# Kernel optimization log

Hardware: AMD Instinct MI355X
Metric: run time of the kernel (lower is better)

## Reference

```python
import jax, jax.numpy as jnp
import numpy as np

N_NODES = 100000
N_EDGES = 1600000
D_IN = 64
D_OUT = 64
BN_EPS = 1e-5


def setup_inputs() -> dict:
    key = jax.random.key(0)
    k1, k2, k3 = jax.random.split(key, 3)
    x = jax.random.normal(k1, (N_NODES, D_IN), dtype=jnp.float32)
    edge_index = jax.random.randint(k2, (2, N_EDGES), 0, N_NODES, dtype=jnp.int64)
    # GCNConv linear weight [out, in], glorot-ish scale
    W = jax.random.normal(k3, (D_OUT, D_IN), dtype=jnp.float32) / np.sqrt(D_IN)
    b = jnp.zeros((D_OUT,), dtype=jnp.float32)
    gamma = jnp.ones((D_OUT,), dtype=jnp.float32)
    beta = jnp.zeros((D_OUT,), dtype=jnp.float32)
    return {"x": x, "edge_index": edge_index, "W": W, "b": b, "gamma": gamma, "beta": beta}


def reference(x, edge_index, W, b, gamma, beta):
    # --- GCNConv: h = x @ W^T, propagate with sym-normalized adjacency + self-loops ---
    h = x @ W.T  # [N, D_OUT]
    src, tgt = edge_index[0], edge_index[1]
    # degree at target nodes, +1 for self-loop
    deg = jax.ops.segment_sum(jnp.ones((src.shape[0],), h.dtype), tgt,
                              num_segments=N_NODES) + 1.0  # [N]
    dinv = jax.lax.rsqrt(deg)
    norm = dinv[src] * dinv[tgt]  # [E]
    # gather -> scale -> scatter-add; self-loop contribution is h / deg
    agg = jax.ops.segment_sum(h[src] * norm[:, None], tgt, num_segments=N_NODES)
    out = agg + h * (1.0 / deg)[:, None] + b  # [N, D_OUT]
    # --- BatchNorm1d (training-mode batch statistics, biased variance) ---
    mean = out.mean(axis=0)
    var = out.var(axis=0)
    y = gamma * (out - mean) * jax.lax.rsqrt(var + BN_EPS) + beta
    # --- ReLU (dropout = identity in eval) ---
    return jax.nn.relu(y)
```

## Files before the change

### kernel.cpp

```cpp
#include <hip/hip_runtime.h>
#include <stdint.h>

#define N_NODES_C 100000
#define N_EDGES_C 1600000
#define DIM 64
#define BN_EPS_C 1e-5f
#define BSH 7
#define NB 782
#define CH 8192

__device__ __forceinline__ int ld_idx(const void* p, int is64, size_t i) {
    if (is64) return (int)((const long long*)p)[i];
    return ((const int*)p)[i];
}

__device__ __forceinline__ float bflo(unsigned int u) {
    return __uint_as_float(u << 16);
}
__device__ __forceinline__ float bfhi(unsigned int u) {
    return __uint_as_float(u & 0xFFFF0000u);
}
__device__ __forceinline__ unsigned short f2bf(float f) {
    unsigned int u = __float_as_uint(f);
    return (unsigned short)((u + 0x7FFF + ((u >> 16) & 1)) >> 16);
}

__global__ void probe_kernel(const unsigned int* __restrict__ p, int* __restrict__ flag) {
    if (threadIdx.x == 0 && blockIdx.x == 0) {
        int is64 = 1;
        for (int i = 1; i < 64; i += 2) {
            if (p[i] != 0u) { is64 = 0; break; }
        }
        *flag = is64;
    }
}

__global__ __launch_bounds__(256) void hist_kernel(const void* __restrict__ ei,
                                                   const int* __restrict__ flag,
                                                   int* __restrict__ bucket_cnt) {
    __shared__ int hist[NB];
    for (int i = threadIdx.x; i < NB; i += 256) hist[i] = 0;
    __syncthreads();
    int is64 = *flag;
    int stride = gridDim.x * blockDim.x;
    for (int e = blockIdx.x * blockDim.x + threadIdx.x; e < N_EDGES_C; e += stride) {
        int tg = ld_idx(ei, is64, (size_t)N_EDGES_C + e);
        atomicAdd(&hist[tg >> BSH], 1);
    }
    __syncthreads();
    for (int i = threadIdx.x; i < NB; i += 256) {
        int c = hist[i];
        if (c) atomicAdd(&bucket_cnt[i], c);
    }
}

__global__ __launch_bounds__(1024) void bucketscan_kernel(const int* __restrict__ bucket_cnt,
                                                          int* __restrict__ bucket_base,
                                                          int* __restrict__ bucket_cursor) {
    __shared__ int s[1024];
    int t = threadIdx.x;
    int v = (t < NB) ? bucket_cnt[t] : 0;
    s[t] = v;
    __syncthreads();
    for (int off = 1; off < 1024; off <<= 1) {
        int u = (t >= off) ? s[t - off] : 0;
        __syncthreads();
        s[t] += u;
        __syncthreads();
    }
    if (t < NB) {
        int excl = s[t] - v;
        bucket_base[t] = excl;
        bucket_cursor[t] = excl;
    }
}

__global__ __launch_bounds__(256) void binscatter_kernel(const void* __restrict__ ei,
                                                         const int* __restrict__ flag,
                                                         int* __restrict__ bucket_cursor,
                                                         unsigned int* __restrict__ csr) {
    __shared__ int hist[NB];
    __shared__ int base[NB];
    int is64 = *flag;
    int e0 = blockIdx.x * CH;
    int eend = min(e0 + CH, N_EDGES_C);
    for (int i = threadIdx.x; i < NB; i += 256) hist[i] = 0;
    __syncthreads();
    for (int e = e0 + threadIdx.x; e < eend; e += 256) {
        int tg = ld_idx(ei, is64, (size_t)N_EDGES_C + e);
        atomicAdd(&hist[tg >> BSH], 1);
    }
    __syncthreads();
    for (int i = threadIdx.x; i < NB; i += 256) {
        int c = hist[i];
        base[i] = c ? atomicAdd(&bucket_cursor[i], c) : 0;
        hist[i] = 0;
    }
    __syncthreads();
    for (int e = e0 + threadIdx.x; e < eend; e += 256) {
        int s  = ld_idx(ei, is64, (size_t)e);
        int tg = ld_idx(ei, is64, (size_t)N_EDGES_C + e);
        int b  = tg >> BSH;
        int tl = tg & 127;
        int pos = base[b] + atomicAdd(&hist[b], 1);
        csr[pos] = ((unsigned int)tl << 17) | (unsigned int)s;
    }
}

__global__ __launch_bounds__(256) void sort_kernel(const unsigned int* __restrict__ csr,
                                                   const int* __restrict__ bucket_base,
                                                   const int* __restrict__ bucket_cnt,
                                                   int* __restrict__ csr2,
                                                   int* __restrict__ rowbase,
                                                   float* __restrict__ dinv) {
    __shared__ int cnt[128];
    __shared__ int sbase[129];
    __shared__ int cur[128];
    int bk = blockIdx.x;
    int t = threadIdx.x;
    if (t < 128) cnt[t] = 0;
    __syncthreads();
    int base = bucket_base[bk], n = bucket_cnt[bk];
    for (int i = t; i < n; i += 256) {
        atomicAdd(&cnt[csr[base + i] >> 17], 1);
    }
    __syncthreads();
    if (t == 0) {
        int run = 0;
        for (int k = 0; k < 128; ++k) { sbase[k] = run; run += cnt[k]; }
        sbase[128] = run;
    }
    __syncthreads();
    if (t < 128) {
        cur[t] = base + sbase[t];
        int node = (bk << BSH) + t;
        if (node < N_NODES_C) {
            rowbase[node] = base + sbase[t];
            float d = (float)(cnt[t] + 1);
            dinv[node] = rsqrtf(d);
        }
    }
    if (bk == 0 && t == 0) rowbase[N_NODES_C] = N_EDGES_C;
    __syncthreads();
    for (int i = t; i < n; i += 256) {
        unsigned int v = csr[base + i];
        int tl = v >> 17;
        int pos = atomicAdd(&cur[tl], 1);
        csr2[pos] = (int)(v & 0x1FFFF);
    }
}

__global__ __launch_bounds__(256) void gemm_kernel(const float* __restrict__ x,
                                                   const float* __restrict__ W,
                                                   const float* __restrict__ dinv,
                                                   unsigned short* __restrict__ hs) {
    __shared__ float Wl[DIM * 65];
    __shared__ float xs[32][DIM];
    int t = threadIdx.x;
    for (int i = t; i < DIM * DIM; i += 256) {
        Wl[(i >> 6) * 65 + (i & 63)] = W[i];
    }
    int r0 = blockIdx.x * 32;
    for (int i = t; i < 32 * DIM; i += 256) {
        int row = i >> 6, col = i & 63;
        int r = r0 + row;
        xs[row][col] = (r < N_NODES_C) ? x[(size_t)r * DIM + col] : 0.0f;
    }
    __syncthreads();
    int wv = t >> 6, c = t & 63;
    for (int it = 0; it < 8; ++it) {
        int rl = it * 4 + wv;
        int r = r0 + rl;
        float acc = 0.0f;
#pragma unroll
        for (int k = 0; k < DIM; ++k) acc += xs[rl][k] * Wl[c * 65 + k];
        if (r < N_NODES_C) hs[(size_t)r * DIM + c] = f2bf(acc * dinv[r]);
    }
}

__global__ __launch_bounds__(256) void gather_kernel(const int* __restrict__ csr2,
                                                     const int* __restrict__ rowbase,
                                                     const float* __restrict__ dinv,
                                                     const unsigned int* __restrict__ hs2,
                                                     const float* __restrict__ b_,
                                                     float2* __restrict__ out,
                                                     float* __restrict__ sums,
                                                     float* __restrict__ sumsq) {
    int lane = threadIdx.x & 63;
    int half = lane >> 5;
    int c2 = lane & 31;
    int wid = blockIdx.x * (blockDim.x >> 6) + (threadIdx.x >> 6);
    int nw = gridDim.x * (blockDim.x >> 6);
    float2 bb = ((const float2*)b_)[c2];
    float s0a = 0.0f, q0a = 0.0f, s1a = 0.0f, q1a = 0.0f;
    for (int p = wid; p < N_NODES_C / 2; p += nw) {
        int t = 2 * p + half;
        int base = rowbase[t];
        int n = rowbase[t + 1] - base;
        float dt = dinv[t];
        float a0 = 0.0f, a1 = 0.0f;
        int j = 0;
        for (; j + 8 <= n; j += 8) {
            int sA = csr2[base + j + 0];
            int sB = csr2[base + j + 1];
            int sC = csr2[base + j + 2];
            int sD = csr2[base + j + 3];
            int sE = csr2[base + j + 4];
            int sF = csr2[base + j + 5];
            int sG = csr2[base + j + 6];
            int sH = csr2[base + j + 7];
            unsigned int uA = hs2[(size_t)sA * 32 + c2];
            unsigned int uB = hs2[(size_t)sB * 32 + c2];
            unsigned int uC = hs2[(size_t)sC * 32 + c2];
            unsigned int uD = hs2[(size_t)sD * 32 + c2];
            unsigned int uE = hs2[(size_t)sE * 32 + c2];
            unsigned int uF = hs2[(size_t)sF * 32 + c2];
            unsigned int uG = hs2[(size_t)sG * 32 + c2];
            unsigned int uH = hs2[(size_t)sH * 32 + c2];
            a0 += bflo(uA); a1 += bfhi(uA);
            a0 += bflo(uB); a1 += bfhi(uB);
            a0 += bflo(uC); a1 += bfhi(uC);
            a0 += bflo(uD); a1 += bfhi(uD);
            a0 += bflo(uE); a1 += bfhi(uE);
            a0 += bflo(uF); a1 += bfhi(uF);
            a0 += bflo(uG); a1 += bfhi(uG);
            a0 += bflo(uH); a1 += bfhi(uH);
        }
        for (; j + 2 <= n; j += 2) {
            int sA = csr2[base + j + 0];
            int sB = csr2[base + j + 1];
            unsigned int uA = hs2[(size_t)sA * 32 + c2];
            unsigned int uB = hs2[(size_t)sB * 32 + c2];
            a0 += bflo(uA); a1 += bfhi(uA);
            a0 += bflo(uB); a1 += bfhi(uB);
        }
        if (j < n) {
            int s = csr2[base + j];
            unsigned int u = hs2[(size_t)s * 32 + c2];
            a0 += bflo(u); a1 += bfhi(u);
        }
        unsigned int ut = hs2[(size_t)t * 32 + c2];
        a0 = fmaf(a0 + bflo(ut), dt, bb.x);
        a1 = fmaf(a1 + bfhi(ut), dt, bb.y);
        out[(size_t)t * 32 + c2] = make_float2(a0, a1);
        s0a += a0; q0a += a0 * a0;
        s1a += a1; q1a += a1 * a1;
    }
    __shared__ float r0[256], r1[256], r2[256], r3[256];
    r0[threadIdx.x] = s0a; r1[threadIdx.x] = q0a;
    r2[threadIdx.x] = s1a; r3[threadIdx.x] = q1a;
    __syncthreads();
    if (threadIdx.x < 32) {
        float S0 = 0, Q0 = 0, S1 = 0, Q1 = 0;
        for (int k = threadIdx.x; k < 256; k += 32) {
            S0 += r0[k]; Q0 += r1[k]; S1 += r2[k]; Q1 += r3[k];
        }
        unsafeAtomicAdd(&sums[2 * threadIdx.x], S0);
        unsafeAtomicAdd(&sums[2 * threadIdx.x + 1], S1);
        unsafeAtomicAdd(&sumsq[2 * threadIdx.x], Q0);
        unsafeAtomicAdd(&sumsq[2 * threadIdx.x + 1], Q1);
    }
}

__global__ void bnparam_kernel(const float* __restrict__ sums,
                               const float* __restrict__ sumsq,
                               const float* __restrict__ gamma,
                               const float* __restrict__ beta,
                               float* __restrict__ scale,
                               float* __restrict__ shift) {
    int c = threadIdx.x;
    if (c < DIM) {
        float m = sums[c] * (1.0f / N_NODES_C);
        float var = sumsq[c] * (1.0f / N_NODES_C) - m * m;
        float sc = gamma[c] * rsqrtf(var + BN_EPS_C);
        scale[c] = sc;
        shift[c] = beta[c] - m * sc;
    }
}

__global__ __launch_bounds__(256) void bnrelu_kernel(float4* __restrict__ out,
                                                     const float* __restrict__ scale,
                                                     const float* __restrict__ shift) {
    const int n4 = N_NODES_C * (DIM / 4);
    int stride = gridDim.x * blockDim.x;
    for (int i = blockIdx.x * blockDim.x + threadIdx.x; i < n4; i += stride) {
        int cb = (i & 15) * 4;
        float4 v = out[i];
        v.x = fmaxf(fmaf(v.x, scale[cb + 0], shift[cb + 0]), 0.0f);
        v.y = fmaxf(fmaf(v.y, scale[cb + 1], shift[cb + 1]), 0.0f);
        v.z = fmaxf(fmaf(v.z, scale[cb + 2], shift[cb + 2]), 0.0f);
        v.w = fmaxf(fmaf(v.w, scale[cb + 3], shift[cb + 3]), 0.0f);
        out[i] = v;
    }
}

extern "C" void kernel_launch(void* const* d_in, const int* in_sizes, int n_in,
                              void* d_out, int out_size, void* d_ws, size_t ws_size,
                              hipStream_t stream) {
    const float* x     = (const float*)d_in[0];
    const void*  ei    = d_in[1];
    const float* W     = (const float*)d_in[2];
    const float* b     = (const float*)d_in[3];
    const float* gamma = (const float*)d_in[4];
    const float* beta  = (const float*)d_in[5];
    float* out = (float*)d_out;

    char* ws = (char*)d_ws;
    int*   flag          = (int*)(ws + 0);
    int*   bucket_cnt    = (int*)(ws + 256);
    int*   bucket_base   = (int*)(ws + 3584);
    int*   bucket_cursor = (int*)(ws + 6912);
    float* dinv          = (float*)(ws + 10240);
    int*   rowbase       = (int*)(ws + 410240);
    float* sums          = (float*)(ws + 810496);
    float* sumsq         = (float*)(ws + 810752);
    float* scale         = (float*)(ws + 811008);
    float* shift         = (float*)(ws + 811264);
    unsigned int* csr    = (unsigned int*)(ws + 811520);
    int*   csr2          = (int*)(ws + 7211520);
    unsigned short* hs   = (unsigned short*)(ws + 13611520);

    hipMemsetAsync(bucket_cnt, 0, NB * sizeof(int), stream);
    hipMemsetAsync(sums, 0, 512, stream);

    probe_kernel<<<1, 64, 0, stream>>>((const unsigned int*)ei, flag);
    hist_kernel<<<256, 256, 0, stream>>>(ei, flag, bucket_cnt);
    bucketscan_kernel<<<1, 1024, 0, stream>>>(bucket_cnt, bucket_base, bucket_cursor);
    binscatter_kernel<<<(N_EDGES_C + CH - 1) / CH, 256, 0, stream>>>(ei, flag,
                                                                    bucket_cursor, csr);
    sort_kernel<<<NB, 256, 0, stream>>>(csr, bucket_base, bucket_cnt, csr2,
                                        rowbase, dinv);
    gemm_kernel<<<(N_NODES_C + 31) / 32, 256, 0, stream>>>(x, W, dinv, hs);
    gather_kernel<<<2048, 256, 0, stream>>>(csr2, rowbase, dinv,
                                            (const unsigned int*)hs, b,
                                            (float2*)out, sums, sumsq);
    bnparam_kernel<<<1, 64, 0, stream>>>(sums, sumsq, gamma, beta, scale, shift);
    bnrelu_kernel<<<1024, 256, 0, stream>>>((float4*)out, scale, shift);
}
```

Baseline: 257.5 us.

## Tile gather by source-node range across rows for cache locality

The sort kernel now sub-buckets each target row's edges into 7 source-node tiles (source>>14), storing per-node tile offsets. Each half-wave of the gather kernel handles 7 consecutive rows and walks all of them tile by tile, so concurrently running waves read source features from the same ~16K-node window and hit cache more often. The workspace layout also changes: csr and hs now share the same memory, which is safe only because the sort kernel consumes csr before the gemm kernel writes hs. In exchange, the gather loops are shorter per tile with more boundary overhead, and the per-node offset array grows to 8 entries per node.

```diff
diff --git a/kernel.cpp b/kernel.cpp
--- a/kernel.cpp
+++ b/kernel.cpp
@@ -8,6 +8,8 @@
 #define BSH 7
 #define NB 782
 #define CH 8192
+#define NT 7
+#define RPS 7
 
 __device__ __forceinline__ int ld_idx(const void* p, int is64, size_t i) {
     if (is64) return (int)((const long long*)p)[i];
@@ -111,41 +113,45 @@
                                                    const int* __restrict__ bucket_base,
                                                    const int* __restrict__ bucket_cnt,
                                                    int* __restrict__ csr2,
-                                                   int* __restrict__ rowbase,
+                                                   int* __restrict__ tilebase,
                                                    float* __restrict__ dinv) {
-    __shared__ int cnt[128];
-    __shared__ int sbase[129];
-    __shared__ int cur[128];
+    __shared__ int cnt[128 * NT];
+    __shared__ int sbase[128 * NT + 1];
+    __shared__ int cur[128 * NT];
     int bk = blockIdx.x;
     int t = threadIdx.x;
-    if (t < 128) cnt[t] = 0;
+    for (int i = t; i < 128 * NT; i += 256) cnt[i] = 0;
     __syncthreads();
     int base = bucket_base[bk], n = bucket_cnt[bk];
     for (int i = t; i < n; i += 256) {
-        atomicAdd(&cnt[csr[base + i] >> 17], 1);
+        unsigned int v = csr[base + i];
+        int key = (int)(v >> 17) * NT + (int)((v & 0x1FFFF) >> 14);
+        atomicAdd(&cnt[key], 1);
     }
     __syncthreads();
     if (t == 0) {
         int run = 0;
-        for (int k = 0; k < 128; ++k) { sbase[k] = run; run += cnt[k]; }
-        sbase[128] = run;
-    }
-    __syncthreads();
+        for (int k = 0; k < 128 * NT; ++k) { sbase[k] = run; run += cnt[k]; }
+        sbase[128 * NT] = run;
+    }
+    __syncthreads();
+    for (int i = t; i < 128 * NT; i += 256) cur[i] = base + sbase[i];
     if (t < 128) {
-        cur[t] = base + sbase[t];
         int node = (bk << BSH) + t;
         if (node < N_NODES_C) {
-            rowbase[node] = base + sbase[t];
-            float d = (float)(cnt[t] + 1);
-            dinv[node] = rsqrtf(d);
-        }
-    }
-    if (bk == 0 && t == 0) rowbase[N_NODES_C] = N_EDGES_C;
+#pragma unroll
+            for (int k = 0; k < NT; ++k)
+                tilebase[node * 8 + k] = base + sbase[t * NT + k];
+            tilebase[node * 8 + NT] = base + sbase[t * NT + NT];
+            int d = sbase[t * NT + NT] - sbase[t * NT];
+            dinv[node] = rsqrtf((float)(d + 1));
+        }
+    }
     __syncthreads();
     for (int i = t; i < n; i += 256) {
         unsigned int v = csr[base + i];
-        int tl = v >> 17;
-        int pos = atomicAdd(&cur[tl], 1);
+        int key = (int)(v >> 17) * NT + (int)((v & 0x1FFFF) >> 14);
+        int pos = atomicAdd(&cur[key], 1);
         csr2[pos] = (int)(v & 0x1FFFF);
     }
 }
@@ -179,7 +185,7 @@
 }
 
 __global__ __launch_bounds__(256) void gather_kernel(const int* __restrict__ csr2,
-                                                     const int* __restrict__ rowbase,
+                                                     const int* __restrict__ tilebase,
                                                      const float* __restrict__ dinv,
                                                      const unsigned int* __restrict__ hs2,
                                                      const float* __restrict__ b_,
@@ -189,62 +195,62 @@
     int lane = threadIdx.x & 63;
     int half = lane >> 5;
     int c2 = lane & 31;
-    int wid = blockIdx.x * (blockDim.x >> 6) + (threadIdx.x >> 6);
-    int nw = gridDim.x * (blockDim.x >> 6);
+    int slot = (blockIdx.x * 4 + (threadIdx.x >> 6)) * 2 + half;
+    int row0 = slot * RPS;
+    float a0[RPS], a1[RPS];
+#pragma unroll
+    for (int r = 0; r < RPS; ++r) { a0[r] = 0.0f; a1[r] = 0.0f; }
+
+    for (int tt = 0; tt < NT; ++tt) {
+        int sr[RPS], er[RPS];
+#pragma unroll
+        for (int r = 0; r < RPS; ++r) {
+            int node = row0 + r;
+            bool valid = node < N_NODES_C;
+            sr[r] = valid ? tilebase[node * 8 + tt] : 0;
+            er[r] = valid ? tilebase[node * 8 + tt + 1] : 0;
+        }
+#pragma unroll
+        for (int r = 0; r < RPS; ++r) {
+            float x0 = a0[r], x1 = a1[r];
+            int j = sr[r], e = er[r];
+            for (; j + 4 <= e; j += 4) {
+                int sA = csr2[j + 0];
+                int sB = csr2[j + 1];
+                int sC = csr2[j + 2];
+                int sD = csr2[j + 3];
+                unsigned int uA = hs2[(size_t)sA * 32 + c2];
+                unsigned int uB = hs2[(size_t)sB * 32 + c2];
+                unsigned int uC = hs2[(size_t)sC * 32 + c2];
+                unsigned int uD = hs2[(size_t)sD * 32 + c2];
+                x0 += bflo(uA); x1 += bfhi(uA);
+                x0 += bflo(uB); x1 += bfhi(uB);
+                x0 += bflo(uC); x1 += bfhi(uC);
+                x0 += bflo(uD); x1 += bfhi(uD);
+            }
+            for (; j < e; ++j) {
+                int s = csr2[j];
+                unsigned int u = hs2[(size_t)s * 32 + c2];
+                x0 += bflo(u); x1 += bfhi(u);
+            }
+            a0[r] = x0; a1[r] = x1;
+        }
+    }
+
     float2 bb = ((const float2*)b_)[c2];
     float s0a = 0.0f, q0a = 0.0f, s1a = 0.0f, q1a = 0.0f;
-    for (int p = wid; p < N_NODES_C / 2; p += nw) {
-        int t = 2 * p + half;
-        int base = rowbase[t];
-        int n = rowbase[t + 1] - base;
-        float dt = dinv[t];
-        float a0 = 0.0f, a1 = 0.0f;
-        int j = 0;
-        for (; j + 8 <= n; j += 8) {
-            int sA = csr2[base + j + 0];
-            int sB = csr2[base + j + 1];
-            int sC = csr2[base + j + 2];
-            int sD = csr2[base + j + 3];
-            int sE = csr2[base + j + 4];
-            int sF = csr2[base + j + 5];
-            int sG = csr2[base + j + 6];
-            int sH = csr2[base + j + 7];
-            unsigned int uA = hs2[(size_t)sA * 32 + c2];
-            unsigned int uB = hs2[(size_t)sB * 32 + c2];
-            unsigned int uC = hs2[(size_t)sC * 32 + c2];
-            unsigned int uD = hs2[(size_t)sD * 32 + c2];
-            unsigned int uE = hs2[(size_t)sE * 32 + c2];
-            unsigned int uF = hs2[(size_t)sF * 32 + c2];
-            unsigned int uG = hs2[(size_t)sG * 32 + c2];
-            unsigned int uH = hs2[(size_t)sH * 32 + c2];
-            a0 += bflo(uA); a1 += bfhi(uA);
-            a0 += bflo(uB); a1 += bfhi(uB);
-            a0 += bflo(uC); a1 += bfhi(uC);
-            a0 += bflo(uD); a1 += bfhi(uD);
-            a0 += bflo(uE); a1 += bfhi(uE);
-            a0 += bflo(uF); a1 += bfhi(uF);
-            a0 += bflo(uG); a1 += bfhi(uG);
-            a0 += bflo(uH); a1 += bfhi(uH);
-        }
-        for (; j + 2 <= n; j += 2) {
-            int sA = csr2[base + j + 0];
-            int sB = csr2[base + j + 1];
-            unsigned int uA = hs2[(size_t)sA * 32 + c2];
-            unsigned int uB = hs2[(size_t)sB * 32 + c2];
-            a0 += bflo(uA); a1 += bfhi(uA);
-            a0 += bflo(uB); a1 += bfhi(uB);
-        }
-        if (j < n) {
-            int s = csr2[base + j];
-            unsigned int u = hs2[(size_t)s * 32 + c2];
-            a0 += bflo(u); a1 += bfhi(u);
-        }
-        unsigned int ut = hs2[(size_t)t * 32 + c2];
-        a0 = fmaf(a0 + bflo(ut), dt, bb.x);
-        a1 = fmaf(a1 + bfhi(ut), dt, bb.y);
-        out[(size_t)t * 32 + c2] = make_float2(a0, a1);
-        s0a += a0; q0a += a0 * a0;
-        s1a += a1; q1a += a1 * a1;
+#pragma unroll
+    for (int r = 0; r < RPS; ++r) {
+        int node = row0 + r;
+        if (node < N_NODES_C) {
+            unsigned int ut = hs2[(size_t)node * 32 + c2];
+            float dt = dinv[node];
+            float v0 = fmaf(a0[r] + bflo(ut), dt, bb.x);
+            float v1 = fmaf(a1[r] + bfhi(ut), dt, bb.y);
+            out[(size_t)node * 32 + c2] = make_float2(v0, v1);
+            s0a += v0; q0a += v0 * v0;
+            s1a += v1; q1a += v1 * v1;
+        }
     }
     __shared__ float r0[256], r1[256], r2[256], r3[256];
     r0[threadIdx.x] = s0a; r1[threadIdx.x] = q0a;
@@ -311,14 +317,14 @@
     int*   bucket_base   = (int*)(ws + 3584);
     int*   bucket_cursor = (int*)(ws + 6912);
     float* dinv          = (float*)(ws + 10240);
-    int*   rowbase       = (int*)(ws + 410240);
-    float* sums          = (float*)(ws + 810496);
-    float* sumsq         = (float*)(ws + 810752);
-    float* scale         = (float*)(ws + 811008);
-    float* shift         = (float*)(ws + 811264);
-    unsigned int* csr    = (unsigned int*)(ws + 811520);
-    int*   csr2          = (int*)(ws + 7211520);
-    unsigned short* hs   = (unsigned short*)(ws + 13611520);
+    int*   tilebase      = (int*)(ws + 410240);
+    float* sums          = (float*)(ws + 3610240);
+    float* sumsq         = (float*)(ws + 3610496);
+    float* scale         = (float*)(ws + 3610752);
+    float* shift         = (float*)(ws + 3611008);
+    int*   csr2          = (int*)(ws + 3611264);
+    unsigned int* csr    = (unsigned int*)(ws + 10011264);
+    unsigned short* hs   = (unsigned short*)(ws + 10011264);
 
     hipMemsetAsync(bucket_cnt, 0, NB * sizeof(int), stream);
     hipMemsetAsync(sums, 0, 512, stream);
@@ -329,9 +335,9 @@
     binscatter_kernel<<<(N_EDGES_C + CH - 1) / CH, 256, 0, stream>>>(ei, flag,
                                                                     bucket_cursor, csr);
     sort_kernel<<<NB, 256, 0, stream>>>(csr, bucket_base, bucket_cnt, csr2,
-                                        rowbase, dinv);
+                                        tilebase, dinv);
     gemm_kernel<<<(N_NODES_C + 31) / 32, 256, 0, stream>>>(x, W, dinv, hs);
-    gather_kernel<<<2048, 256, 0, stream>>>(csr2, rowbase, dinv,
+    gather_kernel<<<2048, 256, 0, stream>>>(csr2, tilebase, dinv,
                                             (const unsigned int*)hs, b,
                                             (float2*)out, sums, sumsq);
     bnparam_kernel<<<1, 64, 0, stream>>>(sums, sumsq, gamma, beta, scale, shift);
```

Result: slower. 297.7 us (+15.6%).
